# Kernel tuning notes

Hardware: AMD Instinct MI355X
Metric: run time of the kernel (lower is better)

Reference implementation:

```python
import jax, jax.numpy as jnp
import numpy as np

B, H, W, C = 32, 32, 32, 512
HEADS, WS, SS = 16, 8, 4
N = WS * WS            # tokens per window
NW = (H // WS) * (W // WS)  # windows per image
HD = C // HEADS
EPS = 1e-5


def _np_window_partition(x, ws):
    b, h, w, c = x.shape
    x = x.reshape(b, h // ws, ws, w // ws, ws, c).transpose(0, 1, 3, 2, 4, 5)
    return x.reshape(-1, ws, ws, c)


def _make_attn_mask():
    img = np.zeros((1, H, W, 1), np.float32)
    sl = (slice(0, -WS), slice(-WS, -SS), slice(-SS, None))
    cnt = 0
    for hs in sl:
        for ws_ in sl:
            img[:, hs, ws_, :] = cnt
            cnt += 1
    mw = _np_window_partition(img, WS).reshape(-1, N)
    d = mw[:, None, :] - mw[:, :, None]
    return np.where(d != 0, np.float32(-100.0), np.float32(0.0))  # [nW, N, N]


def _rel_pos_index():
    coords = np.stack(np.meshgrid(np.arange(WS), np.arange(WS), indexing='ij'))  # [2,ws,ws]
    cf = coords.reshape(2, -1)
    rel = cf[:, :, None] - cf[:, None, :]          # [2,N,N]
    rel = rel.transpose(1, 2, 0)                    # [N,N,2]
    rel[:, :, 0] += WS - 1
    rel[:, :, 1] += WS - 1
    rel[:, :, 0] *= 2 * WS - 1
    return rel.sum(-1)                              # [N,N]

_ATTN_MASK = jnp.asarray(_make_attn_mask())
_RPI = jnp.asarray(_rel_pos_index())


def _ln(x, w, b):
    mu = jnp.mean(x, -1, keepdims=True)
    var = jnp.mean(jnp.square(x - mu), -1, keepdims=True)
    return (x - mu) * jax.lax.rsqrt(var + EPS) * w + b


def _modulate(x, shift, scale):
    return x * (1.0 + scale[:, None, :]) + shift[:, None, :]


def setup_inputs() -> dict:
    key = jax.random.key(0)
    ks = jax.random.split(key, 8)
    s = lambda fan: 1.0 / np.sqrt(fan)
    return {
        'x': jax.random.normal(ks[0], (B, H * W, C), jnp.float32),
        'cond': jax.random.normal(ks[1], (B, C), jnp.float32),
        'norm1_w': jnp.ones((C,), jnp.float32),
        'norm1_b': jnp.zeros((C,), jnp.float32),
        'qkv_w': jax.random.normal(ks[2], (3 * C, C), jnp.float32) * s(C),
        'qkv_b': jnp.zeros((3 * C,), jnp.float32),
        'rpb_table': jax.random.normal(ks[3], ((2 * WS - 1) ** 2, HEADS), jnp.float32) * 0.02,
        'proj_w': jax.random.normal(ks[4], (C, C), jnp.float32) * s(C),
        'proj_b': jnp.zeros((C,), jnp.float32),
        'norm2_w': jnp.ones((C,), jnp.float32),
        'norm2_b': jnp.zeros((C,), jnp.float32),
        'fc1_w': jax.random.normal(ks[5], (4 * C, C), jnp.float32) * s(C),
        'fc1_b': jnp.zeros((4 * C,), jnp.float32),
        'fc2_w': jax.random.normal(ks[6], (C, 4 * C), jnp.float32) * s(4 * C),
        'fc2_b': jnp.zeros((C,), jnp.float32),
        'ada_w': jax.random.normal(ks[7], (6 * C, C), jnp.float32) * s(C),
        'ada_b': jnp.zeros((6 * C,), jnp.float32),
    }


def reference(x, cond, norm1_w, norm1_b, qkv_w, qkv_b, rpb_table, proj_w, proj_b,
              norm2_w, norm2_b, fc1_w, fc1_b, fc2_w, fc2_b, ada_w, ada_b):
    # adaLN modulation params
    ada = jax.nn.silu(cond) @ ada_w.T + ada_b                      # [B, 6C]
    sh_msa, sc_msa, g_msa, sh_mlp, sc_mlp, g_mlp = jnp.split(ada, 6, axis=1)

    shortcut = x
    h = _modulate(_ln(x, norm1_w, norm1_b), sh_msa, sc_msa)        # [B, L, C]
    h = h.reshape(B, H, W, C)
    h = jnp.roll(h, shift=(-SS, -SS), axis=(1, 2))                 # cyclic shift

    # window partition -> [B*nW, N, C]
    hw = h.reshape(B, H // WS, WS, W // WS, WS, C).transpose(0, 1, 3, 2, 4, 5)
    hw = hw.reshape(B * NW, N, C)

    # window attention with relative position bias + shift mask
    qkv = (hw @ qkv_w.T + qkv_b).reshape(B * NW, N, 3, HEADS, HD)
    qkv = qkv.transpose(2, 0, 3, 1, 4)                             # [3, B_, heads, N, hd]
    q, k, v = qkv[0], qkv[1], qkv[2]
    attn = jnp.einsum('bhnd,bhmd->bhnm', q * (HD ** -0.5), k)      # [B_, heads, N, N]
    rpb = rpb_table[_RPI.reshape(-1)].reshape(N, N, HEADS).transpose(2, 0, 1)
    attn = attn + rpb[None]
    attn = attn.reshape(B, NW, HEADS, N, N) + _ATTN_MASK[None, :, None]
    attn = jax.nn.softmax(attn.reshape(B * NW, HEADS, N, N), axis=-1)
    out = jnp.einsum('bhnm,bhmd->bhnd', attn, v)                   # [B_, heads, N, hd]
    out = out.transpose(0, 2, 1, 3).reshape(B * NW, N, C)
    out = out @ proj_w.T + proj_b

    # window reverse -> [B, H, W, C]
    out = out.reshape(B, H // WS, W // WS, WS, WS, C).transpose(0, 1, 3, 2, 4, 5)
    out = out.reshape(B, H, W, C)
    out = jnp.roll(out, shift=(SS, SS), axis=(1, 2)).reshape(B, H * W, C)

    x = shortcut + g_msa[:, None, :] * out

    m = _modulate(_ln(x, norm2_w, norm2_b), sh_mlp, sc_mlp)
    m = jax.nn.gelu(m @ fc1_w.T + fc1_b, approximate=False) @ fc2_w.T + fc2_b
    return x + g_mlp[:, None, :] * m
```

## Files before the change

### kernel.cpp

```cpp
#include <hip/hip_runtime.h>
#include <math.h>

typedef unsigned short u16;
typedef short short8 __attribute__((ext_vector_type(8)));
typedef float floatx4 __attribute__((ext_vector_type(4)));

#define SS 4
#define C_DIM 512
#define L_TOK 1024

static __device__ __forceinline__ u16 f2bf(float f) {
  union { float f; unsigned u; } v; v.f = f;
  unsigned u = v.u;
  unsigned r = (u + 0x7fffu + ((u >> 16) & 1u)) >> 16;
  return (u16)r;
}

typedef const __attribute__((address_space(1))) void* gvp;
typedef __attribute__((address_space(3))) void* lvp;
#define ASYNC16(g, l) __builtin_amdgcn_global_load_lds((gvp)(g), (lvp)(l), 16, 0, 0)

__global__ __launch_bounds__(256) void convert_bf16(const float* __restrict__ src,
                                                    u16* __restrict__ dst, int n4) {
  int i = blockIdx.x * 256 + threadIdx.x;
  if (i >= n4) return;
  float4 v = ((const float4*)src)[i];
  ushort4 o;
  o.x = f2bf(v.x); o.y = f2bf(v.y); o.z = f2bf(v.z); o.w = f2bf(v.w);
  ((ushort4*)dst)[i] = o;
}

__global__ __launch_bounds__(256) void ada_kernel(const float* __restrict__ cond,
                                                  const float* __restrict__ w,
                                                  const float* __restrict__ bias,
                                                  float* __restrict__ ada) {
  int b = blockIdx.y;
  int j = blockIdx.x * 256 + threadIdx.x;
  __shared__ float sc[C_DIM];
  for (int c = threadIdx.x; c < C_DIM; c += 256) {
    float v = cond[b * C_DIM + c];
    sc[c] = v / (1.0f + expf(-v));
  }
  __syncthreads();
  const float* wr = w + (size_t)j * C_DIM;
  float acc = 0.f;
  for (int k = 0; k < C_DIM; k += 4) {
    float4 wv = *(const float4*)&wr[k];
    acc += sc[k] * wv.x + sc[k + 1] * wv.y + sc[k + 2] * wv.z + sc[k + 3] * wv.w;
  }
  ada[(size_t)b * 3072 + j] = acc + bias[j];
}

__global__ __launch_bounds__(64) void prep_attn(const float* __restrict__ rpb,
                                                float* __restrict__ rpbT,
                                                unsigned long long* __restrict__ maskbits) {
  int q = blockIdx.x;
  int head = blockIdx.y;
  int k = threadIdx.x;
  int i1 = q >> 3, j1 = q & 7, i2 = k >> 3, j2 = k & 7;
  rpbT[((size_t)head * 64 + q) * 64 + k] =
      rpb[((i1 - i2 + 7) * 15 + (j1 - j2 + 7)) * 16 + head];
  if (head == 0) {
    for (int widx = 0; widx < 16; widx++) {
      int wh = widx >> 2, wwi = widx & 3;
      int hq = wh * 8 + i1, wq = wwi * 8 + j1;
      int hk = wh * 8 + i2, wk = wwi * 8 + j2;
      int rq = ((hq < 24) ? 0 : (hq < 28) ? 1 : 2) * 3 + ((wq < 24) ? 0 : (wq < 28) ? 1 : 2);
      int rk = ((hk < 24) ? 0 : (hk < 28) ? 1 : 2) * 3 + ((wk < 24) ? 0 : (wk < 28) ? 1 : 2);
      unsigned long long m = __ballot(rq != rk);
      if (k == 0) maskbits[widx * 64 + q] = m;
    }
  }
}

template <int MODE>
__global__ __launch_bounds__(128) void ln_mod(const float* __restrict__ x,
                                              const float* __restrict__ ada,
                                              const float* __restrict__ nw,
                                              const float* __restrict__ nb,
                                              u16* __restrict__ out) {
  int m = blockIdx.x;
  int b = m >> 10;
  size_t srow;
  if (MODE == 0) {
    int n = m & 63, widx = (m >> 6) & 15;
    int wh = widx >> 2, wwi = widx & 3;
    int i = n >> 3, j = n & 7;
    int hs = (wh * 8 + i + SS) & 31;
    int ws_ = (wwi * 8 + j + SS) & 31;
    srow = (size_t)b * L_TOK + hs * 32 + ws_;
  } else {
    srow = (size_t)m;
  }
  const float* src = x + srow * C_DIM;
  int t = threadIdx.x;
  float4 v = *(const float4*)&src[t * 4];
  float s = v.x + v.y + v.z + v.w;
  float ss = v.x * v.x + v.y * v.y + v.z * v.z + v.w * v.w;
#pragma unroll
  for (int off = 32; off > 0; off >>= 1) {
    s += __shfl_down(s, off);
    ss += __shfl_down(ss, off);
  }
  __shared__ float red[4];
  if ((t & 63) == 0) { red[(t >> 6) * 2] = s; red[(t >> 6) * 2 + 1] = ss; }
  __syncthreads();
  float mean = (red[0] + red[2]) * (1.f / C_DIM);
  float var = (red[1] + red[3]) * (1.f / C_DIM) - mean * mean;
  float rstd = rsqrtf(var + 1e-5f);
  const float* sh = ada + (size_t)b * 3072 + (MODE ? 1536 : 0);
  const float* scm = ada + (size_t)b * 3072 + (MODE ? 2048 : 512);
  int c = t * 4;
  ushort4 o;
  {
    float y;
    y = ((v.x - mean) * rstd * nw[c + 0] + nb[c + 0]) * (1.f + scm[c + 0]) + sh[c + 0]; o.x = f2bf(y);
    y = ((v.y - mean) * rstd * nw[c + 1] + nb[c + 1]) * (1.f + scm[c + 1]) + sh[c + 1]; o.y = f2bf(y);
    y = ((v.z - mean) * rstd * nw[c + 2] + nb[c + 2]) * (1.f + scm[c + 2]) + sh[c + 2]; o.z = f2bf(y);
    y = ((v.w - mean) * rstd * nw[c + 3] + nb[c + 3]) * (1.f + scm[c + 3]) + sh[c + 3]; o.w = f2bf(y);
  }
  *(ushort4*)&out[(size_t)m * C_DIM + c] = o;
}

template <int EPI>
__global__ __launch_bounds__(256, 2) void gemm_bf16(
    const u16* __restrict__ A, const u16* __restrict__ Bw,
    const float* __restrict__ bias, int K, int N,
    u16* __restrict__ outBf, float* __restrict__ outF,
    const float* __restrict__ resid, const float* __restrict__ ada) {
  __shared__ __align__(16) u16 lA[2][128 * 32];
  __shared__ __align__(16) u16 lB[2][128 * 32];
  const int tid = threadIdx.x;
  const int lane = tid & 63, wave = tid >> 6;
  const int wr = wave >> 1, wc = wave & 1;
  const int rowA0 = blockIdx.y * 128;
  const int colB0 = blockIdx.x * 128;
  floatx4 acc[4][4];
#pragma unroll
  for (int a = 0; a < 4; a++)
#pragma unroll
    for (int b = 0; b < 4; b++) acc[a][b] = (floatx4){0.f, 0.f, 0.f, 0.f};

  const int r0 = tid >> 2, c0 = (tid & 3) * 8;
  const int q = lane >> 4, fr = lane & 15;

  const u16* gA = &A[(size_t)(rowA0 + r0) * K + c0];
  const u16* gB = &Bw[(size_t)(colB0 + r0) * K + c0];
  const size_t up = (size_t)64 * K;
  u16* lA0 = &lA[0][wave * 512];
  u16* lB0 = &lB[0][wave * 512];

  for (int k0 = 0; k0 < K; k0 += 64) {
    ASYNC16(gA + k0, lA0);
    ASYNC16(gA + k0 + up, lA0 + 2048);
    ASYNC16(gA + k0 + 32, lA0 + 4096);
    ASYNC16(gA + k0 + 32 + up, lA0 + 6144);
    ASYNC16(gB + k0, lB0);
    ASYNC16(gB + k0 + up, lB0 + 2048);
    ASYNC16(gB + k0 + 32, lB0 + 4096);
    ASYNC16(gB + k0 + 32 + up, lB0 + 6144);
    __syncthreads();
#pragma unroll
    for (int kc = 0; kc < 2; kc++) {
      short8 xf[4], wf[4];
#pragma unroll
      for (int mi = 0; mi < 4; mi++)
        xf[mi] = *(const short8*)&lA[kc][(wr * 64 + mi * 16 + fr) * 32 + q * 8];
#pragma unroll
      for (int ni = 0; ni < 4; ni++)
        wf[ni] = *(const short8*)&lB[kc][(wc * 64 + ni * 16 + fr) * 32 + q * 8];
#pragma unroll
      for (int mi = 0; mi < 4; mi++)
#pragma unroll
        for (int ni = 0; ni < 4; ni++)
          acc[mi][ni] = __builtin_amdgcn_mfma_f32_16x16x32_bf16(wf[ni], xf[mi], acc[mi][ni], 0, 0, 0);
    }
    __syncthreads();
  }

#pragma unroll
  for (int mi = 0; mi < 4; mi++) {
    int row = rowA0 + wr * 64 + mi * 16 + fr;
#pragma unroll
    for (int ni = 0; ni < 4; ni++) {
      int col0 = colB0 + wc * 64 + ni * 16 + q * 4;
      float4 bv = *(const float4*)&bias[col0];
      float v0 = acc[mi][ni][0] + bv.x;
      float v1 = acc[mi][ni][1] + bv.y;
      float v2 = acc[mi][ni][2] + bv.z;
      float v3 = acc[mi][ni][3] + bv.w;
      if (EPI == 1) {
        v0 = __fdividef(v0, 1.f + __expf(-v0 * (1.59576912f + 0.07135481f * v0 * v0)));
        v1 = __fdividef(v1, 1.f + __expf(-v1 * (1.59576912f + 0.07135481f * v1 * v1)));
        v2 = __fdividef(v2, 1.f + __expf(-v2 * (1.59576912f + 0.07135481f * v2 * v2)));
        v3 = __fdividef(v3, 1.f + __expf(-v3 * (1.59576912f + 0.07135481f * v3 * v3)));
      }
      if (EPI == 0 || EPI == 1) {
        ushort4 pk;
        pk.x = f2bf(v0); pk.y = f2bf(v1); pk.z = f2bf(v2); pk.w = f2bf(v3);
        *(ushort4*)&outBf[(size_t)row * N + col0] = pk;
      } else if (EPI == 2) {
        int b = row >> 10;
        int n = row & 63, widx = (row >> 6) & 15;
        int wh = widx >> 2, wwi = widx & 3;
        int i = n >> 3, j = n & 7;
        int hd = (wh * 8 + i + SS) & 31;
        int wd = (wwi * 8 + j + SS) & 31;
        size_t dst = ((size_t)b * L_TOK + hd * 32 + wd) * C_DIM + col0;
        float4 rs = *(const float4*)&resid[dst];
        float4 g = *(const float4*)&ada[(size_t)b * 3072 + 1024 + col0];
        float4 o;
        o.x = rs.x + g.x * v0; o.y = rs.y + g.y * v1;
        o.z = rs.z + g.z * v2; o.w = rs.w + g.w * v3;
        *(float4*)&outF[dst] = o;
      } else {
        int b = row >> 10;
        size_t dst = (size_t)row * C_DIM + col0;
        float4 cur = *(const float4*)&outF[dst];
        float4 g = *(const float4*)&ada[(size_t)b * 3072 + 2560 + col0];
        float4 o;
        o.x = cur.x + g.x * v0; o.y = cur.y + g.y * v1;
        o.z = cur.z + g.z * v2; o.w = cur.w + g.w * v3;
        *(float4*)&outF[dst] = o;
      }
    }
  }
}

__global__ __launch_bounds__(256, 2) void attn_mfma(const u16* __restrict__ qkv,
                                                    const float* __restrict__ rpbT,
                                                    const unsigned long long* __restrict__ maskbits,
                                                    u16* __restrict__ out) {
  __shared__ __align__(16) u16 sVT[4][32 * 72];
  __shared__ __align__(16) u16 sP[4][64 * 72];
  const int tid = threadIdx.x, wave = tid >> 6, lane = tid & 63;
  const int col = lane & 15, quad = lane >> 4;
  const int id = blockIdx.x * 4 + wave;
  const int w_ = id >> 4, head = id & 15;
  const int widx = w_ & 15;
  u16* VT = sVT[wave];
  u16* P = sP[wave];
  const u16* base = qkv + (size_t)w_ * 64 * 1536 + head * 32;

  {
    const u16* vrow = base + 1024 + (size_t)lane * 1536;
#pragma unroll
    for (int c = 0; c < 4; c++) {
      uint4 u = *(const uint4*)&vrow[c * 8];
      unsigned uu0 = u.x, uu1 = u.y, uu2 = u.z, uu3 = u.w;
      VT[(c * 8 + 0) * 72 + lane] = (u16)(uu0 & 0xffff);
      VT[(c * 8 + 1) * 72 + lane] = (u16)(uu0 >> 16);
      VT[(c * 8 + 2) * 72 + lane] = (u16)(uu1 & 0xffff);
      VT[(c * 8 + 3) * 72 + lane] = (u16)(uu1 >> 16);
      VT[(c * 8 + 4) * 72 + lane] = (u16)(uu2 & 0xffff);
      VT[(c * 8 + 5) * 72 + lane] = (u16)(uu2 >> 16);
      VT[(c * 8 + 6) * 72 + lane] = (u16)(uu3 & 0xffff);
      VT[(c * 8 + 7) * 72 + lane] = (u16)(uu3 >> 16);
    }
  }

  short8 kf[4], qf[4];
#pragma unroll
  for (int mi = 0; mi < 4; mi++)
    kf[mi] = *(const short8*)(base + 512 + (size_t)(mi * 16 + col) * 1536 + quad * 8);
#pragma unroll
  for (int ni = 0; ni < 4; ni++)
    qf[ni] = *(const short8*)(base + (size_t)(ni * 16 + col) * 1536 + quad * 8);

  floatx4 st[4][4];
#pragma unroll
  for (int mi = 0; mi < 4; mi++)
#pragma unroll
    for (int ni = 0; ni < 4; ni++) st[mi][ni] = (floatx4){0.f, 0.f, 0.f, 0.f};
#pragma unroll
  for (int mi = 0; mi < 4; mi++)
#pragma unroll
    for (int ni = 0; ni < 4; ni++)
      st[mi][ni] = __builtin_amdgcn_mfma_f32_16x16x32_bf16(kf[mi], qf[ni], st[mi][ni], 0, 0, 0);

  const float scale = 0.17677669529663687f;
  float invq[4];
#pragma unroll
  for (int ni = 0; ni < 4; ni++) {
    int q = ni * 16 + col;
    unsigned long long mw = maskbits[widx * 64 + q];
    const float* rp = rpbT + ((size_t)head * 64 + q) * 64;
    float mx = -1e30f;
#pragma unroll
    for (int mi = 0; mi < 4; mi++) {
      floatx4 r4 = *(const floatx4*)&rp[mi * 16 + quad * 4];
#pragma unroll
      for (int r = 0; r < 4; r++) {
        int key = mi * 16 + quad * 4 + r;
        float s = st[mi][ni][r] * scale + r4[r];
        s -= ((mw >> key) & 1ull) ? 100.f : 0.f;
        st[mi][ni][r] = s;
        mx = fmaxf(mx, s);
      }
    }
    mx = fmaxf(mx, __shfl_xor(mx, 16));
    mx = fmaxf(mx, __shfl_xor(mx, 32));
    float sum = 0.f;
#pragma unroll
    for (int mi = 0; mi < 4; mi++) {
      float e0 = __expf(st[mi][ni][0] - mx);
      float e1 = __expf(st[mi][ni][1] - mx);
      float e2 = __expf(st[mi][ni][2] - mx);
      float e3 = __expf(st[mi][ni][3] - mx);
      sum += e0 + e1 + e2 + e3;
      ushort4 pk;
      pk.x = f2bf(e0); pk.y = f2bf(e1); pk.z = f2bf(e2); pk.w = f2bf(e3);
      *(ushort4*)&P[q * 72 + mi * 16 + quad * 4] = pk;
    }
    sum += __shfl_xor(sum, 16);
    sum += __shfl_xor(sum, 32);
    invq[ni] = 1.f / sum;
  }

  floatx4 o[2][4];
#pragma unroll
  for (int mt = 0; mt < 2; mt++)
#pragma unroll
    for (int nt = 0; nt < 4; nt++) o[mt][nt] = (floatx4){0.f, 0.f, 0.f, 0.f};
#pragma unroll
  for (int kc = 0; kc < 2; kc++) {
    short8 vf0 = *(const short8*)&VT[(col) * 72 + kc * 32 + quad * 8];
    short8 vf1 = *(const short8*)&VT[(16 + col) * 72 + kc * 32 + quad * 8];
#pragma unroll
    for (int nt = 0; nt < 4; nt++) {
      short8 pf = *(const short8*)&P[(nt * 16 + col) * 72 + kc * 32 + quad * 8];
      o[0][nt] = __builtin_amdgcn_mfma_f32_16x16x32_bf16(vf0, pf, o[0][nt], 0, 0, 0);
      o[1][nt] = __builtin_amdgcn_mfma_f32_16x16x32_bf16(vf1, pf, o[1][nt], 0, 0, 0);
    }
  }

#pragma unroll
  for (int mt = 0; mt < 2; mt++)
#pragma unroll
    for (int nt = 0; nt < 4; nt++) {
      int q = nt * 16 + col;
      float iv = invq[nt];
      ushort4 pk;
      pk.x = f2bf(o[mt][nt][0] * iv);
      pk.y = f2bf(o[mt][nt][1] * iv);
      pk.z = f2bf(o[mt][nt][2] * iv);
      pk.w = f2bf(o[mt][nt][3] * iv);
      *(ushort4*)&out[((size_t)w_ * 64 + q) * 512 + head * 32 + mt * 16 + quad * 4] = pk;
    }
}

extern "C" void kernel_launch(void* const* d_in, const int* in_sizes, int n_in,
                              void* d_out, int out_size, void* d_ws, size_t ws_size,
                              hipStream_t stream) {
  const float* x      = (const float*)d_in[0];
  const float* cond   = (const float*)d_in[1];
  const float* n1w    = (const float*)d_in[2];
  const float* n1b    = (const float*)d_in[3];
  const float* qkv_w  = (const float*)d_in[4];
  const float* qkv_b  = (const float*)d_in[5];
  const float* rpb    = (const float*)d_in[6];
  const float* proj_w = (const float*)d_in[7];
  const float* proj_b = (const float*)d_in[8];
  const float* n2w    = (const float*)d_in[9];
  const float* n2b    = (const float*)d_in[10];
  const float* fc1_w  = (const float*)d_in[11];
  const float* fc1_b  = (const float*)d_in[12];
  const float* fc2_w  = (const float*)d_in[13];
  const float* fc2_b  = (const float*)d_in[14];
  const float* ada_w  = (const float*)d_in[15];
  const float* ada_b  = (const float*)d_in[16];
  float* out = (float*)d_out;
  char* ws = (char*)d_ws;

  u16*  qkvw_bf  = (u16*)(ws + 0);
  u16*  projw_bf = (u16*)(ws + 1572864);
  u16*  fc1w_bf  = (u16*)(ws + 2097152);
  u16*  fc2w_bf  = (u16*)(ws + 4194304);
  float* ada     = (float*)(ws + 6291456);
  float* rpbT    = (float*)(ws + 6684672);
  unsigned long long* maskb = (unsigned long long*)(ws + 6946816);
  u16*  hw       = (u16*)(ws + 6955008);
  u16*  qkvo     = (u16*)(ws + 40509440);
  u16*  attno    = (u16*)(ws + 141172736);
  u16*  mlp      = (u16*)(ws + 40509440);

  convert_bf16<<<768, 256, 0, stream>>>(qkv_w, qkvw_bf, 196608);
  convert_bf16<<<256, 256, 0, stream>>>(proj_w, projw_bf, 65536);
  convert_bf16<<<1024, 256, 0, stream>>>(fc1_w, fc1w_bf, 262144);
  convert_bf16<<<1024, 256, 0, stream>>>(fc2_w, fc2w_bf, 262144);
  prep_attn<<<dim3(64, 16), 64, 0, stream>>>(rpb, rpbT, maskb);

  ada_kernel<<<dim3(12, 32), 256, 0, stream>>>(cond, ada_w, ada_b, ada);
  ln_mod<0><<<32768, 128, 0, stream>>>(x, ada, n1w, n1b, hw);
  gemm_bf16<0><<<dim3(12, 256), 256, 0, stream>>>(hw, qkvw_bf, qkv_b, 512, 1536,
                                                  qkvo, nullptr, nullptr, nullptr);
  attn_mfma<<<2048, 256, 0, stream>>>(qkvo, rpbT, maskb, attno);
  gemm_bf16<2><<<dim3(4, 256), 256, 0, stream>>>(attno, projw_bf, proj_b, 512, 512,
                                                 nullptr, out, x, ada);
  ln_mod<1><<<32768, 128, 0, stream>>>(out, ada, n2w, n2b, hw);
  gemm_bf16<1><<<dim3(16, 256), 256, 0, stream>>>(hw, fc1w_bf, fc1_b, 512, 2048,
                                                  mlp, nullptr, nullptr, nullptr);
  gemm_bf16<3><<<dim3(4, 256), 256, 0, stream>>>(mlp, fc2w_bf, fc2_b, 2048, 512,
                                                 nullptr, out, nullptr, ada);
}
```

Before: 592.8 us.

## Fuse weight conversions, remap GEMM tiles across XCDs, shrink attention blocks

```diff
diff --git a/kernel.cpp b/kernel.cpp
--- a/kernel.cpp
+++ b/kernel.cpp
@@ -20,14 +20,22 @@
 typedef __attribute__((address_space(3))) void* lvp;
 #define ASYNC16(g, l) __builtin_amdgcn_global_load_lds((gvp)(g), (lvp)(l), 16, 0, 0)
 
-__global__ __launch_bounds__(256) void convert_bf16(const float* __restrict__ src,
-                                                    u16* __restrict__ dst, int n4) {
+__global__ __launch_bounds__(256) void convert_all(const float* __restrict__ s0,
+                                                   const float* __restrict__ s1,
+                                                   const float* __restrict__ s2,
+                                                   const float* __restrict__ s3,
+                                                   u16* __restrict__ d0, u16* __restrict__ d1,
+                                                   u16* __restrict__ d2, u16* __restrict__ d3) {
   int i = blockIdx.x * 256 + threadIdx.x;
-  if (i >= n4) return;
-  float4 v = ((const float4*)src)[i];
+  const float* src; u16* dst; int off;
+  if (i < 196608)      { src = s0; dst = d0; off = i; }
+  else if (i < 262144) { src = s1; dst = d1; off = i - 196608; }
+  else if (i < 524288) { src = s2; dst = d2; off = i - 262144; }
+  else                 { src = s3; dst = d3; off = i - 524288; }
+  float4 v = ((const float4*)src)[off];
   ushort4 o;
   o.x = f2bf(v.x); o.y = f2bf(v.y); o.z = f2bf(v.z); o.w = f2bf(v.w);
-  ((ushort4*)dst)[i] = o;
+  ((ushort4*)dst)[off] = o;
 }
 
 __global__ __launch_bounds__(256) void ada_kernel(const float* __restrict__ cond,
@@ -133,8 +141,12 @@
   const int tid = threadIdx.x;
   const int lane = tid & 63, wave = tid >> 6;
   const int wr = wave >> 1, wc = wave & 1;
-  const int rowA0 = blockIdx.y * 128;
-  const int colB0 = blockIdx.x * 128;
+  const int gx = gridDim.x;
+  const int id = blockIdx.y * gx + blockIdx.x;
+  const int per = (gx * gridDim.y) >> 3;
+  const int nid = (id & 7) * per + (id >> 3);
+  const int rowA0 = (nid / gx) * 128;
+  const int colB0 = (nid % gx) * 128;
   floatx4 acc[4][4];
 #pragma unroll
   for (int a = 0; a < 4; a++)
@@ -227,19 +239,17 @@
   }
 }
 
-__global__ __launch_bounds__(256, 2) void attn_mfma(const u16* __restrict__ qkv,
-                                                    const float* __restrict__ rpbT,
-                                                    const unsigned long long* __restrict__ maskbits,
-                                                    u16* __restrict__ out) {
-  __shared__ __align__(16) u16 sVT[4][32 * 72];
-  __shared__ __align__(16) u16 sP[4][64 * 72];
-  const int tid = threadIdx.x, wave = tid >> 6, lane = tid & 63;
+__global__ __launch_bounds__(64, 4) void attn_mfma(const u16* __restrict__ qkv,
+                                                   const float* __restrict__ rpbT,
+                                                   const unsigned long long* __restrict__ maskbits,
+                                                   u16* __restrict__ out) {
+  __shared__ __align__(16) u16 VT[32 * 72];
+  __shared__ __align__(16) u16 P[64 * 72];
+  const int lane = threadIdx.x;
   const int col = lane & 15, quad = lane >> 4;
-  const int id = blockIdx.x * 4 + wave;
+  const int id = blockIdx.x;
   const int w_ = id >> 4, head = id & 15;
   const int widx = w_ & 15;
-  u16* VT = sVT[wave];
-  u16* P = sP[wave];
   const u16* base = qkv + (size_t)w_ * 64 * 1536 + head * 32;
 
   {
@@ -316,6 +326,7 @@
     sum += __shfl_xor(sum, 32);
     invq[ni] = 1.f / sum;
   }
+  __syncthreads();
 
   floatx4 o[2][4];
 #pragma unroll
@@ -384,17 +395,15 @@
   u16*  attno    = (u16*)(ws + 141172736);
   u16*  mlp      = (u16*)(ws + 40509440);
 
-  convert_bf16<<<768, 256, 0, stream>>>(qkv_w, qkvw_bf, 196608);
-  convert_bf16<<<256, 256, 0, stream>>>(proj_w, projw_bf, 65536);
-  convert_bf16<<<1024, 256, 0, stream>>>(fc1_w, fc1w_bf, 262144);
-  convert_bf16<<<1024, 256, 0, stream>>>(fc2_w, fc2w_bf, 262144);
+  convert_all<<<3072, 256, 0, stream>>>(qkv_w, proj_w, fc1_w, fc2_w,
+                                        qkvw_bf, projw_bf, fc1w_bf, fc2w_bf);
   prep_attn<<<dim3(64, 16), 64, 0, stream>>>(rpb, rpbT, maskb);
 
   ada_kernel<<<dim3(12, 32), 256, 0, stream>>>(cond, ada_w, ada_b, ada);
   ln_mod<0><<<32768, 128, 0, stream>>>(x, ada, n1w, n1b, hw);
   gemm_bf16<0><<<dim3(12, 256), 256, 0, stream>>>(hw, qkvw_bf, qkv_b, 512, 1536,
                                                   qkvo, nullptr, nullptr, nullptr);
-  attn_mfma<<<2048, 256, 0, stream>>>(qkvo, rpbT, maskb, attno);
+  attn_mfma<<<8192, 64, 0, stream>>>(qkvo, rpbT, maskb, attno);
   gemm_bf16<2><<<dim3(4, 256), 256, 0, stream>>>(attno, projw_bf, proj_b, 512, 512,
                                                  nullptr, out, x, ada);
   ln_mod<1><<<32768, 128, 0, stream>>>(out, ada, n2w, n2b, hw);
```

Result: faster. 566.2 us (-4.5%).
